# Kernel tuning notes

Measured on AMD Instinct MI355X. Metric: run time of the kernel, lower is better.

## Reference

```python
import jax, jax.numpy as jnp
import numpy as np

LAT = 4; K = 4; NP = 3 * K - 1; HID = 16; NT = 10; BOUND = 5.0
_in_deg = np.arange(1, LAT + 1)
_hd = (np.arange(HID) % (LAT - 1)) + 1
M1 = jnp.asarray((_hd[:, None] >= _in_deg[None, :]).astype(np.float32))  # [HID, LAT]
M2 = jnp.asarray((_hd[:, None] >= _hd[None, :]).astype(np.float32))      # [HID, HID]
M3 = jnp.asarray((np.repeat(_in_deg, NP)[:, None] > _hd[None, :]).astype(np.float32))  # [LAT*NP, HID]


def _subm(x, m, w, b):
    # submanifold conv: inactive inputs are zero, output restricted to active sites
    y = jax.lax.conv_general_dilated(x, w, (1, 1), 'SAME', dimension_numbers=('NHWC', 'HWIO', 'NHWC')) + b
    return jnp.where(m[..., None], y, 0.0)


def _maxpool(x, m, kh, kw):
    neg = jnp.asarray(-1e30, x.dtype)
    xm = jnp.where(m[..., None], x, neg)
    y = jax.lax.reduce_window(xm, neg, jax.lax.max, (1, kh, kw, 1), (1, kh, kw, 1), 'VALID')
    mo = jax.lax.reduce_window(m.astype(x.dtype), 0.0, jax.lax.max, (1, kh, kw), (1, kh, kw), 'VALID') > 0
    return jnp.where(mo[..., None], y, 0.0), mo


def _invconv(x, w, b, mo):
    # sparse inverse conv with kernel == stride of paired pool: non-overlapping transposed conv
    kh, kw, ci, co = w.shape
    B, h, wd, _ = x.shape
    y = jnp.einsum('bhwc,ijcd->bhiwjd', x, w).reshape(B, h * kh, wd * kw, co) + b
    return jnp.where(mo[..., None], y, 0.0)


def _rqs(x, uw, uh, ud):
    # monotonic rational-quadratic spline, identity outside [-BOUND, BOUND]
    shp = x.shape
    widths = jax.nn.softmax(uw, -1) * (2 * BOUND)
    heights = jax.nn.softmax(uh, -1) * (2 * BOUND)
    edge = jnp.full(shp + (1,), -BOUND, x.dtype)
    xk = jnp.concatenate([edge, jnp.cumsum(widths, -1) - BOUND], -1)
    yk = jnp.concatenate([edge, jnp.cumsum(heights, -1) - BOUND], -1)
    one = jnp.ones(shp + (1,), x.dtype)
    dk = jnp.concatenate([one, jax.nn.softplus(ud), one], -1)
    inside = (x >= -BOUND) & (x <= BOUND)
    xc = jnp.clip(x, -BOUND, BOUND)
    idx = jnp.clip(jnp.sum((xc[..., None] >= xk[..., :-1]).astype(jnp.int32), -1) - 1, 0, K - 1)[..., None]
    g = lambda a, i: jnp.take_along_axis(a, i, -1)[..., 0]
    x0, x1 = g(xk, idx), g(xk, idx + 1)
    y0, y1 = g(yk, idx), g(yk, idx + 1)
    d0, d1 = g(dk, idx), g(dk, idx + 1)
    dx = x1 - x0
    dy = y1 - y0
    s = dy / dx
    t = (xc - x0) / dx
    den = s + (d1 + d0 - 2 * s) * t * (1 - t)
    y = y0 + dy * (s * t * t + d0 * t * (1 - t)) / den
    ld = jnp.log(s * s * (d1 * t * t + 2 * s * t * (1 - t) + d0 * (1 - t) ** 2)) - 2 * jnp.log(den)
    return jnp.where(inside, y, x), jnp.where(inside, ld, 0.0)


def _nsf(z, fW1, fb1, fW2, fb2, fW3, fb3):
    ld_tot = jnp.zeros(z.shape[:-1], z.dtype)
    for t in range(NT):
        h = jax.nn.relu(z @ (fW1[t] * M1).T + fb1[t])
        h = jax.nn.relu(h @ (fW2[t] * M2).T + fb2[t])
        p = (h @ (fW3[t] * M3).T + fb3[t]).reshape(z.shape[:-1] + (LAT, NP))
        z, ld = _rqs(z, p[..., :K], p[..., K:2 * K], p[..., 2 * K:])
        ld_tot = ld_tot + ld.sum(-1)
        if t < NT - 1:
            z = z[..., ::-1]
    return z, ld_tot


def _forward(x, eps, w1, b1, w2, b2, w3, b3, wmu, bmu, wlv, blv, wlin, blin, u1, bu1, w4, b4, u2, bu2, w5, b5, u3, bu3, w6, b6, fW1, fb1, fW2, fb2, fW3, fb3):
    xn = jnp.transpose(x, (0, 2, 3, 1))  # NCHW -> NHWC
    m0 = jnp.any(xn != 0, axis=-1)       # active sites (spconv from_dense)
    lrelu = lambda v: jax.nn.leaky_relu(v, 0.01)
    y = lrelu(_subm(xn, m0, w1, b1))
    y, m1 = _maxpool(y, m0, 2, 2)
    y = lrelu(_subm(y, m1, w2, b2))
    y, m2 = _maxpool(y, m1, 5, 2)
    y = lrelu(_subm(y, m2, w3, b3))
    y, m3 = _maxpool(y, m2, 5, 2)        # [B, 4, 16, 32]
    mu = jnp.where(m3[..., None], y @ wmu.T + bmu, 0.0)
    logvar = jnp.where(m3[..., None], y @ wlv.T + blv, 0.0)
    std = jnp.exp(0.5 * logvar)
    z0 = mu + eps * std
    z, log_det = _nsf(z0, fW1, fb1, fW2, fb2, fW3, fb3)
    LOG2PI = 1.8378770664093453
    log_q0 = jnp.sum(-0.5 * ((z0 - mu) / std) ** 2 - jnp.log(std) - 0.5 * LOG2PI, -1)
    log_p = jnp.sum(-0.5 * z * z - 0.5 * LOG2PI, -1)
    kld_pc = log_q0 - log_det - log_p
    kld = jnp.sum(jnp.where(m3, kld_pc, 0.0), axis=(1, 2))  # index_add over batch indices
    zf = jnp.where(m3[..., None], z, 0.0)
    dec = jnp.where(m3[..., None], zf @ wlin.T + blin, 0.0)
    y = _invconv(dec, u1, bu1, m2)
    y = _subm(y, m2, w4, b4)
    y = _invconv(y, u2, bu2, m1)
    y = _subm(y, m1, w5, b5)
    y = _invconv(y, u3, bu3, m0)
    y = _subm(y, m0, w6, b6)
    out = jnp.transpose(y, (0, 3, 1, 2))  # back to NCHW like .dense()
    return out, mu, logvar, kld, zf


def setup_inputs():
    key = jax.random.key(0)
    ks = iter(jax.random.split(key, 80))
    B, C, H, W = 128, 6, 200, 128
    d = {}
    x = jax.random.normal(next(ks), (B, C, H, W), jnp.float32)
    keep = jax.random.uniform(next(ks), (B, 1, H, W)) < 0.15
    d['x'] = jnp.where(keep, x, 0.0)
    d['eps'] = jax.random.normal(next(ks), (B, 4, 16, LAT), jnp.float32)
    def p(name, shape, s=0.1):
        d[name] = jax.random.normal(next(ks), shape, jnp.float32) * s
    p('w1', (3, 3, 6, 8)); p('b1', (8,))
    p('w2', (3, 3, 8, 16)); p('b2', (16,))
    p('w3', (3, 3, 16, 32)); p('b3', (32,))
    p('wmu', (LAT, 32)); p('bmu', (LAT,))
    p('wlv', (LAT, 32)); p('blv', (LAT,))
    p('wlin', (32, LAT)); p('blin', (32,))
    p('u1', (5, 2, 32, 32)); p('bu1', (32,))
    p('w4', (3, 3, 32, 16)); p('b4', (16,))
    p('u2', (5, 2, 16, 16)); p('bu2', (16,))
    p('w5', (3, 3, 16, 8)); p('b5', (8,))
    p('u3', (2, 2, 8, 8)); p('bu3', (8,))
    p('w6', (3, 3, 8, 6)); p('b6', (6,))
    p('fW1', (NT, HID, LAT)); p('fb1', (NT, HID))
    p('fW2', (NT, HID, HID)); p('fb2', (NT, HID))
    p('fW3', (NT, LAT * NP, HID)); p('fb3', (NT, LAT * NP))
    return d


def reference(x, eps, w1, b1, w2, b2, w3, b3, wmu, bmu, wlv, blv, wlin, blin, u1, bu1, w4, b4, u2, bu2, w5, b5, u3, bu3, w6, b6, fW1, fb1, fW2, fb2, fW3, fb3):
    return _forward(x, eps, w1, b1, w2, b2, w3, b3, wmu, bmu, wlv, blv, wlin, blin, u1, bu1, w4, b4, u2, bu2, w5, b5, u3, bu3, w6, b6, fW1, fb1, fW2, fb2, fW3, fb3)
```

## Files before the change

kernel.cpp:

```cpp
#include <hip/hip_runtime.h>
#include <math.h>

constexpr int NB=128;
constexpr int NH0=200, NW0=128, NC0=6;
constexpr int NH1=100, NW1=64,  NC1=8;
constexpr int NH2=20,  NW2=32,  NC2=16;
constexpr int NH3=4,   NW3=16,  NC3=32;
constexpr int LAT=4, NPp=11, HID=16, NT=10;
constexpr float BOUNDf=5.0f;
constexpr float LOG2PI=1.8378770664093453f;

__device__ __forceinline__ float fexpf(float v){ return __expf(v); }
__device__ __forceinline__ float flogf(float v){ return __logf(v); }
__device__ __forceinline__ float softplusf(float v){ return v>20.f ? v : __logf(1.f+__expf(v)); }
__device__ __forceinline__ float lrelu(float v){ return v>0.f ? v : 0.01f*v; }

__global__ __launch_bounds__(256) void k_conv1pool(
    const float* __restrict__ x, const float* __restrict__ w1, const float* __restrict__ b1,
    float* __restrict__ y1p, unsigned char* __restrict__ m0, unsigned char* __restrict__ m1){
  __shared__ float xs[6][34][34];
  __shared__ float ws1[54][8];
  __shared__ unsigned char ms[34][34];
  int blk = blockIdx.x;
  int b  = blk / 28;
  int t  = blk % 28;
  int th = t / 4, tw = t % 4;
  int hp0 = th*16, wp0 = tw*16;
  int h0 = hp0*2 - 1, w0 = wp0*2 - 1;
  int tid = threadIdx.x;
  for (int i=tid;i<432;i+=256) ws1[i>>3][i&7] = w1[i];
  for (int i=tid;i<6*34*34;i+=256){
    int ci=i/1156; int rem=i-ci*1156; int r=rem/34, c=rem-r*34;
    int h=h0+r, w=w0+c;
    float v=0.f;
    if (h>=0 && h<NH0 && w>=0 && w<NW0) v = x[((size_t)(b*NC0+ci)*NH0+h)*NW0+w];
    xs[ci][r][c]=v;
  }
  __syncthreads();
  for (int i=tid;i<1156;i+=256){
    int r=i/34, c=i-r*34;
    bool any=false;
    #pragma unroll
    for (int ci=0;ci<6;ci++) any |= (xs[ci][r][c]!=0.f);
    ms[r][c] = any?1:0;
  }
  __syncthreads();
  for (int i=tid;i<1024;i+=256){
    int r=(i>>5)+1, c=(i&31)+1;
    int h=h0+r, w=w0+c;
    if (h<NH0) m0[(b*NH0+h)*NW0+w] = ms[r][c];
  }
  int lhp = tid>>4, lwp = tid&15;
  int hp = hp0+lhp, wp = wp0+lwp;
  if (hp < NH1){
    float best[8];
    #pragma unroll
    for (int co=0;co<8;co++) best[co]=-1e30f;
    bool many=false;
    #pragma unroll 1
    for (int i=0;i<2;i++)
    #pragma unroll 1
    for (int j=0;j<2;j++){
      int r = lhp*2+i+1, c = lwp*2+j+1;
      if (!ms[r][c]) continue;
      many=true;
      float a[8];
      #pragma unroll
      for (int co=0;co<8;co++) a[co]=b1[co];
      #pragma unroll 1
      for (int kh=0;kh<3;kh++)
      #pragma unroll 1
      for (int kw=0;kw<3;kw++){
        #pragma unroll
        for (int ci=0;ci<6;ci++){
          float v = xs[ci][r-1+kh][c-1+kw];
          const float* wv = ws1[(kh*3+kw)*6+ci];
          #pragma unroll
          for (int co=0;co<8;co++) a[co]=fmaf(v,wv[co],a[co]);
        }
      }
      #pragma unroll
      for (int co=0;co<8;co++) best[co]=fmaxf(best[co], lrelu(a[co]));
    }
    float* yp = y1p + (((size_t)b*NH1+hp)*NW1+wp)*8;
    #pragma unroll
    for (int co=0;co<8;co++) yp[co] = many?best[co]:0.f;
    m1[(b*NH1+hp)*NW1+wp] = many?1:0;
  }
}

__global__ __launch_bounds__(256) void k_conv2pool(
    const float* __restrict__ yin, const unsigned char* __restrict__ m1,
    const float* __restrict__ w2, const float* __restrict__ b2,
    float* __restrict__ yout, unsigned char* __restrict__ m2){
  __shared__ float ys[8][27][35];
  __shared__ unsigned char msl[27][35];
  __shared__ float w2s[72][16];
  __shared__ float b2s[16];
  int blk = blockIdx.x;
  int b  = blk >> 3;
  int t  = blk & 7;
  int th = t >> 1, tw = t & 1;
  int r0 = th*25 - 1, c0 = tw*32 - 1;
  int tid = threadIdx.x;
  for (int i=tid;i<1152;i+=256) w2s[i>>4][i&15] = w2[i];
  if (tid<16) b2s[tid]=b2[tid];
  for (int p=tid;p<27*34;p+=256){
    int r=p/34, c=p-(p/34)*34;
    int h1=r0+r, w1c=c0+c;
    bool ok = (h1>=0 && h1<NH1 && w1c>=0 && w1c<NW1);
    msl[r][c] = ok ? m1[(b*NH1+h1)*NW1+w1c] : 0;
    float4 v0=make_float4(0,0,0,0), v1=v0;
    if (ok){
      const float4* pp = (const float4*)(yin + (((size_t)b*NH1+h1)*NW1+w1c)*8);
      v0=pp[0]; v1=pp[1];
    }
    ys[0][r][c]=v0.x; ys[1][r][c]=v0.y; ys[2][r][c]=v0.z; ys[3][r][c]=v0.w;
    ys[4][r][c]=v1.x; ys[5][r][c]=v1.y; ys[6][r][c]=v1.z; ys[7][r][c]=v1.w;
  }
  __syncthreads();
  if (tid < 160){
    int oid = tid >> 1, coq = tid & 1;
    int co0 = coq*8;
    int lh = oid >> 4, lw = oid & 15;
    int h2 = th*5+lh, w2c = tw*16+lw;
    float best[8];
    #pragma unroll
    for (int co=0;co<8;co++) best[co]=-1e30f;
    bool many=false;
    #pragma unroll 1
    for (int i=0;i<5;i++)
    #pragma unroll 1
    for (int j=0;j<2;j++){
      int r = lh*5+i+1, c = lw*2+j+1;
      if (!msl[r][c]) continue;
      many=true;
      float a[8];
      #pragma unroll
      for (int co=0;co<8;co++) a[co]=b2s[co0+co];
      #pragma unroll 1
      for (int kh=0;kh<3;kh++)
      #pragma unroll 1
      for (int kw=0;kw<3;kw++){
        #pragma unroll
        for (int ci=0;ci<8;ci++){
          float v = ys[ci][r-1+kh][c-1+kw];
          const float* wr = w2s[(kh*3+kw)*8+ci];
          #pragma unroll
          for (int co=0;co<8;co++) a[co]=fmaf(v,wr[co0+co],a[co]);
        }
      }
      #pragma unroll
      for (int co=0;co<8;co++) best[co]=fmaxf(best[co], lrelu(a[co]));
    }
    float4 o0,o1;
    if (many){
      o0=make_float4(best[0],best[1],best[2],best[3]);
      o1=make_float4(best[4],best[5],best[6],best[7]);
    } else { o0=make_float4(0,0,0,0); o1=o0; }
    float4* op = (float4*)(yout + (((size_t)b*NH2+h2)*NW2+w2c)*16 + co0);
    op[0]=o0; op[1]=o1;
    if (coq==0) m2[(b*NH2+h2)*NW2+w2c] = many?1:0;
  }
}

__global__ __launch_bounds__(256) void k_conv3pool(
    const float* __restrict__ yin, const unsigned char* __restrict__ m2,
    const float* __restrict__ w3, const float* __restrict__ b3,
    float* __restrict__ yout, unsigned char* __restrict__ m3,
    float* __restrict__ out_kld){
  __shared__ float ys[16][20][33];
  __shared__ unsigned char msl[20][32];
  __shared__ float w3s[144][32];
  __shared__ float b3s[32];
  int b = blockIdx.x;
  int tid = threadIdx.x;
  if (tid==0) out_kld[b]=0.f;
  for (int i=tid;i<4608;i+=256) w3s[i>>5][i&31] = w3[i];
  if (tid<32) b3s[tid]=b3[tid];
  for (int p=tid;p<640;p+=256){
    int r=p>>5, c=p&31;
    msl[r][c] = m2[(b*NH2+r)*NW2+c];
    const float4* pp = (const float4*)(yin + (((size_t)b*NH2+r)*NW2+c)*16);
    float4 q0=pp[0],q1=pp[1],q2=pp[2],q3=pp[3];
    ys[0][r][c]=q0.x; ys[1][r][c]=q0.y; ys[2][r][c]=q0.z; ys[3][r][c]=q0.w;
    ys[4][r][c]=q1.x; ys[5][r][c]=q1.y; ys[6][r][c]=q1.z; ys[7][r][c]=q1.w;
    ys[8][r][c]=q2.x; ys[9][r][c]=q2.y; ys[10][r][c]=q2.z; ys[11][r][c]=q2.w;
    ys[12][r][c]=q3.x; ys[13][r][c]=q3.y; ys[14][r][c]=q3.z; ys[15][r][c]=q3.w;
  }
  __syncthreads();
  int p = tid>>2, coq = tid&3;
  int co0 = coq*8;
  int hp = p>>4, wp = p&15;
  float best[8];
  #pragma unroll
  for (int co=0;co<8;co++) best[co]=-1e30f;
  bool many=false;
  #pragma unroll 1
  for (int i=0;i<5;i++)
  #pragma unroll 1
  for (int j=0;j<2;j++){
    int h2 = hp*5+i, w2c = wp*2+j;
    if (!msl[h2][w2c]) continue;
    many=true;
    float a[8];
    #pragma unroll
    for (int co=0;co<8;co++) a[co]=b3s[co0+co];
    #pragma unroll 1
    for (int kh=0;kh<3;kh++){
      int hh=h2+kh-1;
      if (hh<0||hh>=NH2) continue;
      #pragma unroll 1
      for (int kw=0;kw<3;kw++){
        int ww=w2c+kw-1;
        if (ww<0||ww>=NW2) continue;
        #pragma unroll
        for (int ci=0;ci<16;ci++){
          float v = ys[ci][hh][ww];
          const float* wr = w3s[(kh*3+kw)*16+ci];
          #pragma unroll
          for (int co=0;co<8;co++) a[co]=fmaf(v,wr[co0+co],a[co]);
        }
      }
    }
    #pragma unroll
    for (int co=0;co<8;co++) best[co]=fmaxf(best[co], lrelu(a[co]));
  }
  float4 o0,o1;
  if (many){
    o0=make_float4(best[0],best[1],best[2],best[3]);
    o1=make_float4(best[4],best[5],best[6],best[7]);
  } else { o0=make_float4(0,0,0,0); o1=o0; }
  float4* op = (float4*)(yout + ((size_t)(b*64+p))*32 + co0);
  op[0]=o0; op[1]=o1;
  if (coq==0) m3[b*64+p] = many?1:0;
}

__global__ __launch_bounds__(64) void k_latent(
    const float* __restrict__ y3p, const unsigned char* __restrict__ m3,
    const float* __restrict__ eps,
    const float* __restrict__ wmu, const float* __restrict__ bmu,
    const float* __restrict__ wlv, const float* __restrict__ blv,
    const float* __restrict__ wlin, const float* __restrict__ blin,
    const float* __restrict__ fW1, const float* __restrict__ fb1,
    const float* __restrict__ fW2, const float* __restrict__ fb2,
    const float* __restrict__ fW3, const float* __restrict__ fb3,
    float* __restrict__ out_mu, float* __restrict__ out_lv,
    float* __restrict__ out_kld, float* __restrict__ out_zf,
    float* __restrict__ dec)
{
  __shared__ __align__(16) float sW1[NT*HID*LAT];
  __shared__ float sb1[NT*HID];
  __shared__ __align__(16) float sW2[NT*HID*HID];
  __shared__ float sb2[NT*HID];
  __shared__ __align__(16) float sW3[NT*LAT*NPp*HID];
  __shared__ float sb3[NT*LAT*NPp];
  __shared__ __align__(16) float swmu[LAT*NC3];
  __shared__ __align__(16) float swlv[LAT*NC3];
  __shared__ __align__(16) float slin[NC3*LAT];
  __shared__ float sbmu[LAT], sblv[LAT], sblin[NC3];
  int tid = threadIdx.x;
  for (int i=tid;i<NT*HID*LAT;i+=64){ int j=i&3; int r=(i>>2)%HID; sW1[i]=fW1[i]*(((r%3+1)>=(j+1))?1.f:0.f); }
  for (int i=tid;i<NT*HID;i+=64){ sb1[i]=fb1[i]; sb2[i]=fb2[i]; }
  for (int i=tid;i<NT*HID*HID;i+=64){ int j=i&15; int r=(i>>4)%HID; sW2[i]=fW2[i]*(((r%3+1)>=(j%3+1))?1.f:0.f); }
  for (int i=tid;i<NT*LAT*NPp*HID;i+=64){ int j=i&15; int r=(i>>4)%(LAT*NPp); sW3[i]=fW3[i]*(((r/NPp+1)>(j%3+1))?1.f:0.f); }
  for (int i=tid;i<NT*LAT*NPp;i+=64) sb3[i]=fb3[i];
  for (int i=tid;i<LAT*NC3;i+=64){ swmu[i]=wmu[i]; swlv[i]=wlv[i]; slin[i]=wlin[i]; }
  if (tid<LAT){ sbmu[tid]=bmu[tid]; sblv[tid]=blv[tid]; }
  for (int i=tid;i<NC3;i+=64) sblin[i]=blin[i];
  __syncthreads();

  int blk = blockIdx.x;
  int b   = blk >> 2;
  int gpos = b*64 + (blk&3)*16 + (tid>>2);
  int g = tid & 3;
  bool msk = m3[gpos]!=0;
  float kld_part = 0.f;
  if (msk){
    const float4* yp = (const float4*)(y3p + (size_t)gpos*NC3);
    const float4* wm = (const float4*)(swmu + g*NC3);
    const float4* wl = (const float4*)(swlv + g*NC3);
    float mu_g = sbmu[g], lv_g = sblv[g];
    #pragma unroll
    for (int q=0;q<8;q++){
      float4 yq = yp[q], a = wm[q], c = wl[q];
      mu_g = fmaf(yq.x,a.x, fmaf(yq.y,a.y, fmaf(yq.z,a.z, fmaf(yq.w,a.w, mu_g))));
      lv_g = fmaf(yq.x,c.x, fmaf(yq.y,c.y, fmaf(yq.z,c.z, fmaf(yq.w,c.w, lv_g))));
    }
    float std_g = fexpf(0.5f*lv_g);
    float ev_g  = eps[(size_t)gpos*LAT+g];
    float z0_g  = fmaf(ev_g, std_g, mu_g);
    float zg = z0_g;
    float z[4];
    z[g]=zg; z[g^1]=__shfl_xor(zg,1); z[g^2]=__shfl_xor(zg,2); z[g^3]=__shfl_xor(zg,3);
    float ld_g = 0.f;
    for (int t=0;t<NT;t++){
      float h1[16];
      const float4* W1t = (const float4*)(sW1 + t*HID*LAT);
      const float*  b1t = sb1 + t*HID;
      #pragma unroll
      for (int i2=0;i2<16;i2++){
        float4 w = W1t[i2];
        float a = b1t[i2];
        a = fmaf(z[0],w.x, fmaf(z[1],w.y, fmaf(z[2],w.z, fmaf(z[3],w.w, a))));
        h1[i2]=fmaxf(a,0.f);
      }
      float h2o[4];
      const float* W2t = sW2 + t*HID*HID;
      const float* b2t = sb2 + t*HID;
      #pragma unroll
      for (int k=0;k<4;k++){
        int row = g*4+k;
        const float4* wr = (const float4*)(W2t + row*HID);
        float a = b2t[row];
        #pragma unroll
        for (int q=0;q<4;q++){
          float4 w = wr[q];
          a = fmaf(h1[q*4+0],w.x, fmaf(h1[q*4+1],w.y, fmaf(h1[q*4+2],w.z, fmaf(h1[q*4+3],w.w, a))));
        }
        h2o[k]=fmaxf(a,0.f);
      }
      float h2[16];
      #pragma unroll
      for (int k=0;k<4;k++) h2[g*4+k]=h2o[k];
      #pragma unroll
      for (int mski=1;mski<4;mski++){
        int og = g^mski;
        #pragma unroll
        for (int k=0;k<4;k++) h2[og*4+k]=__shfl_xor(h2o[k],mski);
      }
      float p[NPp];
      const float* W3t = sW3 + t*LAT*NPp*HID;
      const float* b3t = sb3 + t*LAT*NPp;
      #pragma unroll
      for (int r=0;r<NPp;r++){
        int row = g*NPp+r;
        const float4* wr = (const float4*)(W3t + row*HID);
        float a = b3t[row];
        #pragma unroll
        for (int q=0;q<4;q++){
          float4 w = wr[q];
          a = fmaf(h2[q*4+0],w.x, fmaf(h2[q*4+1],w.y, fmaf(h2[q*4+2],w.z, fmaf(h2[q*4+3],w.w, a))));
        }
        p[r]=a;
      }
      float mw=fmaxf(fmaxf(p[0],p[1]),fmaxf(p[2],p[3]));
      float e0=fexpf(p[0]-mw), e1=fexpf(p[1]-mw), e2=fexpf(p[2]-mw), e3=fexpf(p[3]-mw);
      float wsc=10.f/(e0+e1+e2+e3);
      float xk1=fmaf(e0,wsc,-BOUNDf), xk2=fmaf(e1,wsc,xk1), xk3=fmaf(e2,wsc,xk2), xk4=fmaf(e3,wsc,xk3);
      float mh=fmaxf(fmaxf(p[4],p[5]),fmaxf(p[6],p[7]));
      float f0=fexpf(p[4]-mh), f1=fexpf(p[5]-mh), f2=fexpf(p[6]-mh), f3=fexpf(p[7]-mh);
      float hsc=10.f/(f0+f1+f2+f3);
      float yk1=fmaf(f0,hsc,-BOUNDf), yk2=fmaf(f1,hsc,yk1), yk3=fmaf(f2,hsc,yk2), yk4=fmaf(f3,hsc,yk3);
      float dk1=softplusf(p[8]), dk2=softplusf(p[9]), dk3=softplusf(p[10]);
      float xv=z[g];
      bool inside = (xv>=-BOUNDf)&&(xv<=BOUNDf);
      float xc=fminf(fmaxf(xv,-BOUNDf),BOUNDf);
      float x0=-BOUNDf, x1=xk1, y0=-BOUNDf, y1=yk1, d0=1.f, d1=dk1;
      if (xc>=xk1){x0=xk1;x1=xk2;y0=yk1;y1=yk2;d0=dk1;d1=dk2;}
      if (xc>=xk2){x0=xk2;x1=xk3;y0=yk2;y1=yk3;d0=dk2;d1=dk3;}
      if (xc>=xk3){x0=xk3;x1=xk4;y0=yk3;y1=yk4;d0=dk3;d1=1.f;}
      float dxv=x1-x0, dyv=y1-y0;
      float sl=dyv/dxv, ttv=(xc-x0)/dxv, omt=1.f-ttv;
      float den=sl + (d1+d0-2.f*sl)*ttv*omt;
      float yo=y0 + dyv*(sl*ttv*ttv + d0*ttv*omt)/den;
      float ldv=flogf(sl*sl*(d1*ttv*ttv + 2.f*sl*ttv*omt + d0*omt*omt)) - 2.f*flogf(den);
      float zn_g = inside ? yo : xv;
      ld_g += inside ? ldv : 0.f;
      float znf[4];
      znf[g]=zn_g; znf[g^1]=__shfl_xor(zn_g,1); znf[g^2]=__shfl_xor(zn_g,2); znf[g^3]=__shfl_xor(zn_g,3);
      if (t<NT-1){ z[0]=znf[3]; z[1]=znf[2]; z[2]=znf[1]; z[3]=znf[0]; }
      else       { z[0]=znf[0]; z[1]=znf[1]; z[2]=znf[2]; z[3]=znf[3]; }
    }
    float lq_g = -0.5f*ev_g*ev_g - 0.5f*lv_g - 0.5f*LOG2PI;
    float lp_g = -0.5f*z[g]*z[g] - 0.5f*LOG2PI;
    kld_part = lq_g - ld_g - lp_g;
    out_mu[(size_t)gpos*LAT+g]=mu_g;
    out_lv[(size_t)gpos*LAT+g]=lv_g;
    out_zf[(size_t)gpos*LAT+g]=z[g];
    float4 d0v, d1v;
    {
      float dv[8];
      #pragma unroll
      for (int k=0;k<8;k++){
        int c = g*8+k;
        const float4 w = ((const float4*)slin)[c];
        dv[k] = fmaf(z[0],w.x, fmaf(z[1],w.y, fmaf(z[2],w.z, fmaf(z[3],w.w, sblin[c]))));
      }
      d0v=make_float4(dv[0],dv[1],dv[2],dv[3]);
      d1v=make_float4(dv[4],dv[5],dv[6],dv[7]);
    }
    float4* dp = (float4*)(dec + (size_t)gpos*NC3 + g*8);
    dp[0]=d0v; dp[1]=d1v;
  } else {
    out_mu[(size_t)gpos*LAT+g]=0.f;
    out_lv[(size_t)gpos*LAT+g]=0.f;
    out_zf[(size_t)gpos*LAT+g]=0.f;
    float4 zv = make_float4(0,0,0,0);
    float4* dp = (float4*)(dec + (size_t)gpos*NC3 + g*8);
    dp[0]=zv; dp[1]=zv;
  }
  float s = kld_part;
  s += __shfl_xor(s,1);  s += __shfl_xor(s,2);
  s += __shfl_xor(s,4);  s += __shfl_xor(s,8);
  s += __shfl_xor(s,16); s += __shfl_xor(s,32);
  if (tid==0) atomicAdd(&out_kld[b], s);
}

__global__ __launch_bounds__(256) void k_ic4(
    const float* __restrict__ dec, const unsigned char* __restrict__ m2,
    const float* __restrict__ u1, const float* __restrict__ bu1,
    const float* __restrict__ w4, const float* __restrict__ b4,
    float* __restrict__ t2){
  __shared__ __align__(16) float vs[12][18][32];
  __shared__ __align__(16) float w4s[288][16];
  __shared__ unsigned char msl[12][18];
  int blk = blockIdx.x;
  int b  = blk >> 2;
  int t  = blk & 3;
  int th = t >> 1, tw = t & 1;
  int h0 = th*10, w0 = tw*16;
  int tid = threadIdx.x;
  for (int i=tid;i<288*16;i+=256) w4s[i>>4][i&15] = w4[i];
  if (tid < 216){
    int lr = tid/18, lc = tid%18;
    int h2 = h0-1+lr, w2 = w0-1+lc;
    bool mk = (h2>=0 && h2<NH2 && w2>=0 && w2<NW2) && m2[(b*NH2+h2)*NW2+w2];
    msl[lr][lc] = mk?1:0;
    float acc[32];
    if (mk){
      const float* dp = dec + (((size_t)b*NH3 + h2/5)*NW3 + w2/2)*NC3;
      const float* up = u1 + ((h2%5)*2 + (w2&1))*1024;
      #pragma unroll
      for (int co=0;co<32;co++) acc[co]=bu1[co];
      #pragma unroll 1
      for (int ci=0;ci<32;ci++){
        float dv = dp[ci];
        const float* ur = up + ci*32;
        #pragma unroll
        for (int co=0;co<32;co++) acc[co]=fmaf(dv,ur[co],acc[co]);
      }
    } else {
      #pragma unroll
      for (int co=0;co<32;co++) acc[co]=0.f;
    }
    #pragma unroll
    for (int co=0;co<32;co++) vs[lr][lc][co]=acc[co];
  }
  __syncthreads();
  if (tid < 160){
    int lh = tid/16, lw = tid%16;
    int h2 = h0+lh, w2 = w0+lw;
    float a[16];
    if (msl[lh+1][lw+1]){
      #pragma unroll
      for (int co=0;co<16;co++) a[co]=b4[co];
      #pragma unroll 1
      for (int kh=0;kh<3;kh++)
      #pragma unroll 1
      for (int kw=0;kw<3;kw++){
        const float* vp = vs[lh+kh][lw+kw];
        #pragma unroll
        for (int ci=0;ci<32;ci++){
          float v = vp[ci];
          const float* wr = w4s[(kh*3+kw)*32+ci];
          #pragma unroll
          for (int co=0;co<16;co++) a[co]=fmaf(v,wr[co],a[co]);
        }
      }
    } else {
      #pragma unroll
      for (int co=0;co<16;co++) a[co]=0.f;
    }
    float* op = t2 + (((size_t)b*NH2+h2)*NW2+w2)*NC2;
    #pragma unroll
    for (int co=0;co<16;co++) op[co]=a[co];
  }
}

__global__ __launch_bounds__(256) void k_ic5(
    const float* __restrict__ t2, const unsigned char* __restrict__ m1,
    const float* __restrict__ u2, const float* __restrict__ bu2,
    const float* __restrict__ w5, const float* __restrict__ b5,
    float* __restrict__ t4){
  __shared__ __align__(16) float vs[12][18][16];
  __shared__ __align__(16) float w5s[144][8];
  __shared__ unsigned char msl[12][18];
  int blk = blockIdx.x;
  int b  = blk / 40;
  int t  = blk % 40;
  int th = t >> 2, tw = t & 3;
  int h0 = th*10, w0 = tw*16;
  int tid = threadIdx.x;
  for (int i=tid;i<144*8;i+=256) w5s[i>>3][i&7] = w5[i];
  if (tid < 216){
    int lr = tid/18, lc = tid%18;
    int h1 = h0-1+lr, w1c = w0-1+lc;
    bool mk = (h1>=0 && h1<NH1 && w1c>=0 && w1c<NW1) && m1[(b*NH1+h1)*NW1+w1c];
    msl[lr][lc] = mk?1:0;
    float acc[16];
    if (mk){
      const float* dp = t2 + (((size_t)b*NH2 + h1/5)*NW2 + w1c/2)*NC2;
      const float* up = u2 + ((h1%5)*2 + (w1c&1))*256;
      #pragma unroll
      for (int co=0;co<16;co++) acc[co]=bu2[co];
      #pragma unroll 1
      for (int ci=0;ci<16;ci++){
        float dv = dp[ci];
        const float* ur = up + ci*16;
        #pragma unroll
        for (int co=0;co<16;co++) acc[co]=fmaf(dv,ur[co],acc[co]);
      }
    } else {
      #pragma unroll
      for (int co=0;co<16;co++) acc[co]=0.f;
    }
    #pragma unroll
    for (int co=0;co<16;co++) vs[lr][lc][co]=acc[co];
  }
  __syncthreads();
  if (tid < 160){
    int lh = tid/16, lw = tid%16;
    int h1 = h0+lh, w1c = w0+lw;
    float a[8];
    if (msl[lh+1][lw+1]){
      #pragma unroll
      for (int co=0;co<8;co++) a[co]=b5[co];
      #pragma unroll 1
      for (int kh=0;kh<3;kh++)
      #pragma unroll 1
      for (int kw=0;kw<3;kw++){
        const float* vp = vs[lh+kh][lw+kw];
        #pragma unroll
        for (int ci=0;ci<16;ci++){
          float v = vp[ci];
          const float* wr = w5s[(kh*3+kw)*16+ci];
          #pragma unroll
          for (int co=0;co<8;co++) a[co]=fmaf(v,wr[co],a[co]);
        }
      }
    } else {
      #pragma unroll
      for (int co=0;co<8;co++) a[co]=0.f;
    }
    float* op = t4 + (((size_t)b*NH1+h1)*NW1+w1c)*NC1;
    #pragma unroll
    for (int co=0;co<8;co++) op[co]=a[co];
  }
}

__global__ __launch_bounds__(256) void k_inv3conv6(
    const float* __restrict__ t4, const unsigned char* __restrict__ m0,
    const float* __restrict__ u3, const float* __restrict__ bu3,
    const float* __restrict__ w6, const float* __restrict__ b6,
    float* __restrict__ out){
  __shared__ float ts[8][10][36];
  __shared__ unsigned char msl[18][66];
  __shared__ float u3s[4][8][8];
  __shared__ float w6s[9][8][6];
  __shared__ float bu3s[8];
  __shared__ float b6s[6];
  int blk = blockIdx.x;
  int b  = blk / 26;
  int t  = blk % 26;
  int th = t >> 1, tw = t & 1;
  int h0 = th*16, w0 = tw*64;
  int base_r = 8*th - 1, base_c = 32*tw - 1;
  int tid = threadIdx.x;
  for (int i=tid;i<256;i+=256){ int pos=i>>6; int rem=i&63; u3s[pos][rem>>3][rem&7]=u3[i]; }
  for (int i=tid;i<432;i+=256){ int tap=i/48; int rem=i%48; w6s[tap][rem/6][rem%6]=w6[i]; }
  if (tid<8) bu3s[tid]=bu3[tid];
  if (tid<6) b6s[tid]=b6[tid];
  for (int p=tid;p<340;p+=256){
    int r=p/34, c=p-(p/34)*34;
    int h1=base_r+r, w1c=base_c+c;
    float4 v0=make_float4(0,0,0,0), v1=v0;
    if (h1>=0 && h1<NH1 && w1c>=0 && w1c<NW1){
      const float4* pp = (const float4*)(t4 + (((size_t)b*NH1+h1)*NW1+w1c)*8);
      v0=pp[0]; v1=pp[1];
    }
    ts[0][r][c]=v0.x; ts[1][r][c]=v0.y; ts[2][r][c]=v0.z; ts[3][r][c]=v0.w;
    ts[4][r][c]=v1.x; ts[5][r][c]=v1.y; ts[6][r][c]=v1.z; ts[7][r][c]=v1.w;
  }
  for (int p=tid;p<18*66;p+=256){
    int r=p/66, c=p-(p/66)*66;
    int h=h0-1+r, w=w0-1+c;
    msl[r][c] = (h>=0 && h<NH0 && w>=0 && w<NW0) ? m0[(b*NH0+h)*NW0+w] : 0;
  }
  __syncthreads();
  #pragma unroll 1
  for (int k=0;k<4;k++){
    int p = tid + k*256;
    int lh = p>>6, lw = p&63;
    int h = h0+lh, w = w0+lw;
    if (h >= NH0) continue;
    float acc[6];
    if (msl[lh+1][lw+1]){
      #pragma unroll
      for (int co=0;co<6;co++) acc[co]=b6s[co];
      #pragma unroll 1
      for (int kh=0;kh<3;kh++)
      #pragma unroll 1
      for (int kw=0;kw<3;kw++){
        if (!msl[lh+kh][lw+kw]) continue;
        int hh = h+kh-1, ww = w+kw-1;
        int tr = (hh>>1) - base_r, tc = (ww>>1) - base_c;
        int pos = (hh&1)*2 + (ww&1);
        float v8[8];
        #pragma unroll
        for (int c8=0;c8<8;c8++) v8[c8]=bu3s[c8];
        #pragma unroll
        for (int ci=0;ci<8;ci++){
          float v = ts[ci][tr][tc];
          #pragma unroll
          for (int c8=0;c8<8;c8++) v8[c8]=fmaf(v, u3s[pos][ci][c8], v8[c8]);
        }
        const float (*wt)[6] = w6s[kh*3+kw];
        #pragma unroll
        for (int ci=0;ci<8;ci++)
          #pragma unroll
          for (int co=0;co<6;co++) acc[co]=fmaf(v8[ci], wt[ci][co], acc[co]);
      }
    } else {
      #pragma unroll
      for (int co=0;co<6;co++) acc[co]=0.f;
    }
    size_t base = (size_t)b*6*NH0*NW0 + (size_t)h*NW0 + w;
    #pragma unroll
    for (int co=0;co<6;co++) out[base + (size_t)co*NH0*NW0] = acc[co];
  }
}

extern "C" void kernel_launch(void* const* d_in, const int* in_sizes, int n_in,
                              void* d_out, int out_size, void* d_ws, size_t ws_size,
                              hipStream_t stream){
  (void)in_sizes; (void)n_in; (void)out_size; (void)ws_size;
  const float* x    = (const float*)d_in[0];
  const float* eps  = (const float*)d_in[1];
  const float* w1   = (const float*)d_in[2];
  const float* b1   = (const float*)d_in[3];
  const float* w2   = (const float*)d_in[4];
  const float* b2   = (const float*)d_in[5];
  const float* w3   = (const float*)d_in[6];
  const float* b3   = (const float*)d_in[7];
  const float* wmu  = (const float*)d_in[8];
  const float* bmu  = (const float*)d_in[9];
  const float* wlv  = (const float*)d_in[10];
  const float* blv  = (const float*)d_in[11];
  const float* wlin = (const float*)d_in[12];
  const float* blin = (const float*)d_in[13];
  const float* u1   = (const float*)d_in[14];
  const float* bu1  = (const float*)d_in[15];
  const float* w4   = (const float*)d_in[16];
  const float* b4   = (const float*)d_in[17];
  const float* u2   = (const float*)d_in[18];
  const float* bu2  = (const float*)d_in[19];
  const float* w5   = (const float*)d_in[20];
  const float* b5   = (const float*)d_in[21];
  const float* u3   = (const float*)d_in[22];
  const float* bu3  = (const float*)d_in[23];
  const float* w6   = (const float*)d_in[24];
  const float* b6   = (const float*)d_in[25];
  const float* fW1  = (const float*)d_in[26];
  const float* fb1  = (const float*)d_in[27];
  const float* fW2  = (const float*)d_in[28];
  const float* fb2  = (const float*)d_in[29];
  const float* fW3  = (const float*)d_in[30];
  const float* fb3  = (const float*)d_in[31];

  char* ws = (char*)d_ws;
  unsigned char* m0 = (unsigned char*)(ws);
  unsigned char* m1 = (unsigned char*)(ws + 3276800);
  unsigned char* m2 = (unsigned char*)(ws + 4096000);
  unsigned char* m3 = (unsigned char*)(ws + 4177920);
  float* y1p = (float*)(ws + 4194304);
  float* y2p = (float*)(ws + 30408704);
  float* y3p = (float*)(ws + 35651584);
  float* dec = (float*)(ws + 36700160);
  float* t2  = y2p;
  float* t4  = y1p;

  float* out   = (float*)d_out;
  float* o_mu  = out + 19660800;
  float* o_lv  = out + 19693568;
  float* o_kld = out + 19726336;
  float* o_zf  = out + 19726464;

  k_conv1pool<<< 3584,256,0,stream>>>(x, w1, b1, y1p, m0, m1);
  k_conv2pool<<< 1024,256,0,stream>>>(y1p, m1, w2, b2, y2p, m2);
  k_conv3pool<<<  128,256,0,stream>>>(y2p, m2, w3, b3, y3p, m3, o_kld);
  k_latent   <<<  512, 64,0,stream>>>(y3p, m3, eps, wmu,bmu,wlv,blv,wlin,blin,
                                      fW1,fb1,fW2,fb2,fW3,fb3, o_mu,o_lv,o_kld,o_zf, dec);
  k_ic4      <<<  512,256,0,stream>>>(dec, m2, u1, bu1, w4, b4, t2);
  k_ic5      <<< 5120,256,0,stream>>>(t2, m1, u2, bu2, w5, b5, t4);
  k_inv3conv6<<< 3328,256,0,stream>>>(t4, m0, u3, bu3, w6, b6, out);
}
```

Measured before the change: 482.0 us.

## Precompute inverse-conv outputs into shared tile before final conv

The last kernel used to recompute the 8-channel inverse-conv (u3) value for each of the 9 taps of every output pixel. It now computes each halo pixel's u3 output once, stores it in a shared-memory tile (zeroed at inactive sites), and the 3x3 conv reads that tile directly. This removes roughly ninefold redundant FMAs and the per-tap mask branches. The cost is a larger shared tile (about 39KB), which may reduce occupancy, plus an extra barrier.

```diff
diff --git a/kernel.cpp b/kernel.cpp
--- a/kernel.cpp
+++ b/kernel.cpp
@@ -554,7 +554,7 @@
     const float* __restrict__ u3, const float* __restrict__ bu3,
     const float* __restrict__ w6, const float* __restrict__ b6,
     float* __restrict__ out){
-  __shared__ float ts[8][10][36];
+  __shared__ float vs[8][18][68];
   __shared__ unsigned char msl[18][66];
   __shared__ float u3s[4][8][8];
   __shared__ float w6s[9][8][6];
@@ -565,27 +565,37 @@
   int t  = blk % 26;
   int th = t >> 1, tw = t & 1;
   int h0 = th*16, w0 = tw*64;
-  int base_r = 8*th - 1, base_c = 32*tw - 1;
   int tid = threadIdx.x;
-  for (int i=tid;i<256;i+=256){ int pos=i>>6; int rem=i&63; u3s[pos][rem>>3][rem&7]=u3[i]; }
+  for (int i=tid;i<256;i+=256){ u3s[i>>6][(i>>3)&7][i&7]=u3[i]; }
   for (int i=tid;i<432;i+=256){ int tap=i/48; int rem=i%48; w6s[tap][rem/6][rem%6]=w6[i]; }
   if (tid<8) bu3s[tid]=bu3[tid];
   if (tid<6) b6s[tid]=b6[tid];
-  for (int p=tid;p<340;p+=256){
-    int r=p/34, c=p-(p/34)*34;
-    int h1=base_r+r, w1c=base_c+c;
-    float4 v0=make_float4(0,0,0,0), v1=v0;
-    if (h1>=0 && h1<NH1 && w1c>=0 && w1c<NW1){
-      const float4* pp = (const float4*)(t4 + (((size_t)b*NH1+h1)*NW1+w1c)*8);
-      v0=pp[0]; v1=pp[1];
-    }
-    ts[0][r][c]=v0.x; ts[1][r][c]=v0.y; ts[2][r][c]=v0.z; ts[3][r][c]=v0.w;
-    ts[4][r][c]=v1.x; ts[5][r][c]=v1.y; ts[6][r][c]=v1.z; ts[7][r][c]=v1.w;
-  }
+  __syncthreads();
   for (int p=tid;p<18*66;p+=256){
     int r=p/66, c=p-(p/66)*66;
     int h=h0-1+r, w=w0-1+c;
-    msl[r][c] = (h>=0 && h<NH0 && w>=0 && w<NW0) ? m0[(b*NH0+h)*NW0+w] : 0;
+    bool act = (h>=0 && h<NH0 && w>=0 && w<NW0) && m0[(b*NH0+h)*NW0+w];
+    msl[r][c] = act?1:0;
+    float v8[8];
+    if (act){
+      const float4* tp = (const float4*)(t4 + (((size_t)b*NH1 + (h>>1))*NW1 + (w>>1))*8);
+      float4 q0=tp[0], q1=tp[1];
+      float tin[8]={q0.x,q0.y,q0.z,q0.w,q1.x,q1.y,q1.z,q1.w};
+      const float (*up)[8] = u3s[(h&1)*2+(w&1)];
+      #pragma unroll
+      for (int c8=0;c8<8;c8++) v8[c8]=bu3s[c8];
+      #pragma unroll
+      for (int ci=0;ci<8;ci++){
+        float v=tin[ci];
+        #pragma unroll
+        for (int c8=0;c8<8;c8++) v8[c8]=fmaf(v, up[ci][c8], v8[c8]);
+      }
+    } else {
+      #pragma unroll
+      for (int c8=0;c8<8;c8++) v8[c8]=0.f;
+    }
+    #pragma unroll
+    for (int c8=0;c8<8;c8++) vs[c8][r][c]=v8[c8];
   }
   __syncthreads();
   #pragma unroll 1
@@ -602,24 +612,13 @@
       for (int kh=0;kh<3;kh++)
       #pragma unroll 1
       for (int kw=0;kw<3;kw++){
-        if (!msl[lh+kh][lw+kw]) continue;
-        int hh = h+kh-1, ww = w+kw-1;
-        int tr = (hh>>1) - base_r, tc = (ww>>1) - base_c;
-        int pos = (hh&1)*2 + (ww&1);
-        float v8[8];
-        #pragma unroll
-        for (int c8=0;c8<8;c8++) v8[c8]=bu3s[c8];
+        const float (*wt)[6] = w6s[kh*3+kw];
         #pragma unroll
         for (int ci=0;ci<8;ci++){
-          float v = ts[ci][tr][tc];
+          float v = vs[ci][lh+kh][lw+kw];
           #pragma unroll
-          for (int c8=0;c8<8;c8++) v8[c8]=fmaf(v, u3s[pos][ci][c8], v8[c8]);
-        }
-        const float (*wt)[6] = w6s[kh*3+kw];
-        #pragma unroll
-        for (int ci=0;ci<8;ci++)
-          #pragma unroll
-          for (int co=0;co<6;co++) acc[co]=fmaf(v8[ci], wt[ci][co], acc[co]);
+          for (int co=0;co<6;co++) acc[co]=fmaf(v, wt[ci][co], acc[co]);
+        }
       }
     } else {
       #pragma unroll
```

Result: faster. 454.4 us (-5.7%).
